# Optimization experiments

Measured on AMD Instinct MI355X. Metric: run time of the kernel, lower is better.

Reference implementation:

```python
import jax, jax.numpy as jnp
import numpy as np

B, S, D, H, FF = 2, 2048, 1024, 16, 4096
DK = D // H
MAX_SEQ_LEN = 2048
THETA = 10000.0
EPS = 1e-5


def _linear_init(key, out_f, in_f):
    std = (2.0 / (in_f + out_f)) ** 0.5
    return std * jax.random.truncated_normal(key, -3.0, 3.0, (out_f, in_f), dtype=jnp.float32)


def setup_inputs() -> dict:
    key = jax.random.key(0)
    ks = jax.random.split(key, 9)
    x = jax.random.normal(ks[0], (B, S, D), dtype=jnp.float32)
    token_positions = jnp.broadcast_to(jnp.arange(S, dtype=jnp.int32)[None, :], (B, S))
    return {
        "x": x,
        "wq": _linear_init(ks[1], D, D),
        "wk": _linear_init(ks[2], D, D),
        "wv": _linear_init(ks[3], D, D),
        "wo": _linear_init(ks[4], D, D),
        "w1": _linear_init(ks[5], FF, D),
        "w2": _linear_init(ks[6], D, FF),
        "w3": _linear_init(ks[7], FF, D),
        "g1": jnp.ones((D,), dtype=jnp.float32),
        "g2": jnp.ones((D,), dtype=jnp.float32),
        "token_positions": token_positions,
    }


def _rmsnorm(x, g):
    x32 = x.astype(jnp.float32)
    ms = jnp.sqrt(jnp.mean(x32 * x32, axis=-1, keepdims=True) + EPS)
    return ((x32 / ms) * g).astype(x.dtype)


def _rope(x, pos):
    # x: (B, H, S, DK); pos: (B, S)
    inv_freq = 1.0 / THETA ** (jnp.arange(0, DK, 2, dtype=jnp.float32) / DK)  # (DK/2,)
    freqs = pos.astype(jnp.float32)[..., None] * inv_freq  # (B, S, DK/2)
    cos = jnp.cos(freqs)[:, None, :, :]  # (B, 1, S, DK/2) broadcast over heads
    sin = jnp.sin(freqs)[:, None, :, :]
    x_real = x[..., 0::2]
    x_imag = x[..., 1::2]
    rot_real = x_real * cos - x_imag * sin
    rot_imag = x_real * sin + x_imag * cos
    return jnp.stack([rot_real, rot_imag], axis=-1).reshape(x.shape)


def reference(x, wq, wk, wv, wo, w1, w2, w3, g1, g2, token_positions):
    # --- attention sublayer ---
    h = _rmsnorm(x, g1)
    def proj(w):
        y = jnp.einsum('bsd,ed->bse', h, w)
        return y.reshape(B, S, H, DK).transpose(0, 2, 1, 3)  # (B,H,S,DK)
    Q = _rope(proj(wq), token_positions)
    K = _rope(proj(wk), token_positions)
    V = proj(wv)
    scores = jnp.einsum('bhqd,bhkd->bhqk', Q, K)  # (B,H,S,S) full matrix (naive)
    causal = jnp.tril(jnp.ones((S, S), dtype=bool))
    scores = jnp.where(causal, scores, -jnp.inf) / (DK ** 0.5)
    probs = jax.nn.softmax(scores, axis=-1)
    attn = jnp.einsum('bhqk,bhkd->bhqd', probs, V)
    attn = attn.transpose(0, 2, 1, 3).reshape(B, S, D)
    attn = jnp.einsum('bsd,ed->bse', attn, wo)
    y = x + attn
    # --- SwiGLU FFN sublayer ---
    h2 = _rmsnorm(y, g2)
    a = jnp.einsum('bsd,fd->bsf', h2, w1)
    gate = jnp.einsum('bsd,fd->bsf', h2, w3)
    ff = jnp.einsum('bsf,df->bsd', a * jax.nn.sigmoid(a) * gate, w2)
    return y + ff
```

## Files before the change

kernel.cpp:

```cpp
#include <hip/hip_runtime.h>
#include <hip/hip_bf16.h>

#define B_ 2
#define S_ 2048
#define D_ 1024
#define H_ 16
#define DK_ 64
#define FF_ 4096
#define M_ (B_ * S_)

typedef unsigned short u16;
typedef __bf16 bf16x8 __attribute__((ext_vector_type(8)));
typedef float f32x4 __attribute__((ext_vector_type(4)));
typedef u16 u16x4 __attribute__((ext_vector_type(4)));
typedef u16 u16x8 __attribute__((ext_vector_type(8)));

__device__ __forceinline__ u16 f2bf(float f) {
  __bf16 b = (__bf16)f;
  return __builtin_bit_cast(u16, b);
}
__device__ __forceinline__ float bf2f(u16 u) {
  __bf16 b = __builtin_bit_cast(__bf16, u);
  return (float)b;
}

__device__ __forceinline__ void async_lds16(const void* g, void* l) {
  __builtin_amdgcn_global_load_lds(
      (const __attribute__((address_space(1))) unsigned int*)g,
      (__attribute__((address_space(3))) unsigned int*)l, 16, 0, 0);
}

__global__ __launch_bounds__(256) void f2b_all(
    const float* __restrict__ wq, const float* __restrict__ wk,
    const float* __restrict__ wv, const float* __restrict__ wo,
    const float* __restrict__ w1, const float* __restrict__ w2,
    const float* __restrict__ w3, u16* __restrict__ wqkvb,
    u16* __restrict__ wob, u16* __restrict__ w1b, u16* __restrict__ w2b,
    u16* __restrict__ w3b) {
  int i4 = blockIdx.x * 256 + threadIdx.x;
  const float* src;
  u16* dst;
  int off;
  if (i4 < 262144) { src = wq; dst = wqkvb; off = i4; }
  else if (i4 < 524288) { src = wk; dst = wqkvb + 1048576; off = i4 - 262144; }
  else if (i4 < 786432) { src = wv; dst = wqkvb + 2097152; off = i4 - 524288; }
  else if (i4 < 1048576) { src = wo; dst = wob; off = i4 - 786432; }
  else if (i4 < 2097152) { src = w1; dst = w1b; off = i4 - 1048576; }
  else if (i4 < 3145728) { src = w2; dst = w2b; off = i4 - 2097152; }
  else { src = w3; dst = w3b; off = i4 - 3145728; }
  float4 v = ((const float4*)src)[off];
  u16x4 o;
  o[0] = f2bf(v.x); o[1] = f2bf(v.y); o[2] = f2bf(v.z); o[3] = f2bf(v.w);
  *(u16x4*)(dst + (size_t)off * 4) = o;
}

__global__ __launch_bounds__(256) void rmsnorm_k(const float* __restrict__ X,
                                                 const float* __restrict__ G,
                                                 u16* __restrict__ Out) {
  const int row = blockIdx.x, tid = threadIdx.x;
  const float4 xv = *(const float4*)(X + (size_t)row * D_ + tid * 4);
  float ss = xv.x * xv.x + xv.y * xv.y + xv.z * xv.z + xv.w * xv.w;
#pragma unroll
  for (int off = 1; off < 64; off <<= 1) ss += __shfl_xor(ss, off);
  __shared__ float red[4];
  if ((tid & 63) == 0) red[tid >> 6] = ss;
  __syncthreads();
  const float tot = red[0] + red[1] + red[2] + red[3];
  const float sc = rsqrtf(tot * (1.0f / D_) + 1e-5f);
  const float4 gv = *(const float4*)(G + tid * 4);
  u16x4 o;
  o[0] = f2bf(xv.x * sc * gv.x);
  o[1] = f2bf(xv.y * sc * gv.y);
  o[2] = f2bf(xv.z * sc * gv.z);
  o[3] = f2bf(xv.w * sc * gv.w);
  *(u16x4*)(Out + (size_t)row * D_ + tid * 4) = o;
}

__global__ __launch_bounds__(256) void rope2_k(unsigned int* __restrict__ Qb,
                                               unsigned int* __restrict__ Kb,
                                               const int* __restrict__ pos) {
  int idx = blockIdx.x * 256 + threadIdx.x;
  unsigned int* buf = Qb;
  float scale = 0.125f;
  if (idx >= 2097152) { buf = Kb; scale = 1.f; idx -= 2097152; }
  const int row = idx >> 9, p = idx & 511;
  const int i = p & 31;
  unsigned int v = buf[(size_t)row * 512 + p];
  const float xr = bf2f((u16)(v & 0xffffu));
  const float xi = bf2f((u16)(v >> 16));
  const float ang =
      (float)pos[row] * __expf(-(float)i * (9.210340371976184f / 32.0f));
  float sn, cs;
  sincosf(ang, &sn, &cs);
  const float orr = (xr * cs - xi * sn) * scale;
  const float oii = (xr * sn + xi * cs) * scale;
  buf[(size_t)row * 512 + p] =
      (unsigned int)f2bf(orr) | ((unsigned int)f2bf(oii) << 16);
}

__global__ __launch_bounds__(256) void transpose_v(const u16* __restrict__ V,
                                                   u16* __restrict__ Vt) {
  __shared__ __align__(16) u16 tile[32][64];
  const int tid = threadIdx.x;
  const int s0 = blockIdx.x * 32, bh = blockIdx.y, b = bh >> 4, h = bh & 15;
  {
    const int sr = tid >> 3, c = tid & 7;
    *(u16x8*)&tile[sr][c * 8] =
        *(const u16x8*)(V + (size_t)(b * S_ + s0 + sr) * D_ + h * DK_ + c * 8);
  }
  __syncthreads();
  {
    const int dk = tid >> 2, cs = tid & 3;
    u16x8 vv;
#pragma unroll
    for (int j = 0; j < 8; ++j) vv[j] = tile[cs * 8 + j][dk];
    *(u16x8*)(Vt + (size_t)(bh * DK_ + dk) * S_ + s0 + cs * 8) = vv;
  }
}

template <int BM, int BN, int BK, int EPI>
__global__ __launch_bounds__(512) void gemm2ph(const u16* __restrict__ A,
                                               const u16* __restrict__ Bw,
                                               void* __restrict__ Cout,
                                               const void* __restrict__ auxp,
                                               int N, int K) {
  constexpr int CPR = BK / 8;
  constexpr int ACH = BM * CPR;
  constexpr int TCH = (BM + BN) * CPR;
  constexpr int MR = BM / 32, NR = BN / 64;
  __shared__ __align__(16) u16 As[2][BM * BK];
  __shared__ __align__(16) u16 Bs[2][BN * BK];
  const int tid = threadIdx.x, l = tid & 63, w = tid >> 6;
  const int gx = gridDim.x;
  const int nwg = gx * (int)gridDim.y;
  const int id = blockIdx.y * gx + blockIdx.x;
  const int swz = (id & 7) * (nwg >> 3) + (id >> 3);
  const int m0 = (swz / gx) * BM, n0 = (swz % gx) * BN;
  const int wm = (w >> 2) * (BM / 2), wn = (w & 3) * (BN / 4);
  const int lr = l & 15, lg = l >> 4;

  f32x4 acc[MR][NR] = {};

  auto STAGE = [&](int bf, int k0) {
#pragma unroll
    for (int i = 0; i < TCH / 512; ++i) {
      const int s = i * 512 + tid;
      const int base = i * 512 + w * 64;
      if (base < ACH) {
        const int r = s / CPR, ch = s % CPR;
        async_lds16(A + (size_t)(m0 + r) * K + k0 + ((ch ^ (r & 7)) * 8),
                    (char*)As[bf] + base * 16);
      } else {
        const int s2 = s - ACH;
        const int r = s2 / CPR, ch = s2 % CPR;
        async_lds16(Bw + (size_t)(n0 + r) * K + k0 + ((ch ^ (r & 7)) * 8),
                    (char*)Bs[bf] + (base - ACH) * 16);
      }
    }
  };

  STAGE(0, 0);
  __syncthreads();
  int cur = 0;
  for (int k0 = 0; k0 < K; k0 += BK) {
    if (k0 + BK < K) STAGE(cur ^ 1, k0 + BK);
#pragma unroll
    for (int kk = 0; kk < BK / 32; ++kk) {
      bf16x8 af[MR], bfr[NR];
#pragma unroll
      for (int i = 0; i < MR; ++i) {
        const int row = wm + i * 16 + lr;
        af[i] = *(const bf16x8*)&As[cur][row * BK +
                                         (((kk * 4 + lg) ^ (row & 7)) * 8)];
      }
#pragma unroll
      for (int j = 0; j < NR; ++j) {
        const int row = wn + j * 16 + lr;
        bfr[j] = *(const bf16x8*)&Bs[cur][row * BK +
                                          (((kk * 4 + lg) ^ (row & 7)) * 8)];
      }
      __builtin_amdgcn_s_setprio(1);
#pragma unroll
      for (int i = 0; i < MR; ++i)
#pragma unroll
        for (int j = 0; j < NR; ++j)
          acc[i][j] = __builtin_amdgcn_mfma_f32_16x16x32_bf16(
              af[i], bfr[j], acc[i][j], 0, 0, 0);
      __builtin_amdgcn_s_setprio(0);
    }
    __syncthreads();
    cur ^= 1;
  }

#pragma unroll
  for (int i = 0; i < MR; ++i) {
#pragma unroll
    for (int j = 0; j < NR; ++j) {
#pragma unroll
      for (int t = 0; t < 4; ++t) {
        const int grow = m0 + wm + i * 16 + lg * 4 + t;
        const int gcol = n0 + wn + j * 16 + lr;
        const float v = acc[i][j][t];
        if (EPI == 0) {
          ((u16*)Cout)[(size_t)grow * N + gcol] = f2bf(v);
        } else if (EPI == 1) {
          const size_t idx = (size_t)grow * N + gcol;
          ((float*)Cout)[idx] = ((const float*)auxp)[idx] + v;
        } else if (EPI == 2) {
          const size_t idx = (size_t)grow * N + gcol;
          const float av = bf2f(((const u16*)auxp)[idx]);
          const float sw = av / (1.f + __expf(-av));
          ((u16*)Cout)[idx] = f2bf(sw * v);
        } else {
          u16* base = (u16*)Cout + (size_t)(gcol >> 10) * ((size_t)M_ * D_);
          base[(size_t)grow * D_ + (gcol & 1023)] = f2bf(v);
        }
      }
    }
  }
}

__global__ __launch_bounds__(256) void attn_fwd(const u16* __restrict__ Q,
                                                const u16* __restrict__ K,
                                                const u16* __restrict__ Vt,
                                                u16* __restrict__ O) {
  __shared__ __align__(16) u16 Ks[2][64 * 64];
  __shared__ __align__(16) u16 Vs[2][64 * 64];
  __shared__ __align__(16) u16 Ps[4][16 * 72];
  const int tid = threadIdx.x, l = tid & 63, w = tid >> 6;
  const int lr = l & 15, lg = l >> 4;
  const int bid = blockIdx.x;
  const int xcd = bid & 7, i = bid >> 3;
  const int bh = xcd * 4 + (i >> 5);
  const int qx = 31 - (i & 31);
  const int b = bh >> 4, h = bh & 15;
  const int q0w = qx * 64 + w * 16;

  const u16* Kb = K + (size_t)(b * S_) * D_ + h * DK_;
  const u16* Vb = Vt + (size_t)bh * DK_ * S_;

  bf16x8 aq[2];
  {
    const u16* qp = Q + (size_t)(b * S_ + q0w + lr) * D_ + h * DK_ + lg * 8;
    aq[0] = *(const bf16x8*)qp;
    aq[1] = *(const bf16x8*)(qp + 32);
  }
  f32x4 oacc[4] = {};
  float mrow[4], lrow[4];
#pragma unroll
  for (int t = 0; t < 4; ++t) { mrow[t] = -1e30f; lrow[t] = 0.f; }

  auto STAGE = [&](int bf, int t) {
#pragma unroll
    for (int inst = 0; inst < 2; ++inst) {
      const int s = (w * 2 + inst) * 64 + l;
      const int r = s >> 3, ch = s & 7;
      const int chs = ch ^ (r & 7);
      async_lds16(Kb + (size_t)(t * 64 + r) * D_ + chs * 8,
                  (char*)Ks[bf] + (w * 2 + inst) * 1024);
      async_lds16(Vb + (size_t)r * S_ + t * 64 + chs * 8,
                  (char*)Vs[bf] + (w * 2 + inst) * 1024);
    }
  };

  auto QKT = [&](int cur, f32x4* sf) {
    __builtin_amdgcn_s_setprio(1);
#pragma unroll
    for (int n = 0; n < 4; ++n) {
      const int kvr = n * 16 + lr;
      f32x4 z = {};
#pragma unroll
      for (int ss = 0; ss < 2; ++ss) {
        const int cw = ss * 4 + lg;
        bf16x8 bk = *(const bf16x8*)&Ks[cur][kvr * 64 + ((cw ^ (kvr & 7)) * 8)];
        z = __builtin_amdgcn_mfma_f32_16x16x32_bf16(aq[ss], bk, z, 0, 0, 0);
      }
      sf[n] = z;
    }
    __builtin_amdgcn_s_setprio(0);
  };

  auto PV = [&](int cur) {
    bf16x8 ap0 = *(const bf16x8*)&Ps[w][lr * 72 + lg * 8];
    bf16x8 ap1 = *(const bf16x8*)&Ps[w][lr * 72 + 32 + lg * 8];
    __builtin_amdgcn_s_setprio(1);
#pragma unroll
    for (int d = 0; d < 4; ++d) {
      const int row = d * 16 + lr;
      bf16x8 bv0 = *(const bf16x8*)&Vs[cur][row * 64 + ((lg ^ (row & 7)) * 8)];
      bf16x8 bv1 =
          *(const bf16x8*)&Vs[cur][row * 64 + (((4 + lg) ^ (row & 7)) * 8)];
      oacc[d] = __builtin_amdgcn_mfma_f32_16x16x32_bf16(ap0, bv0, oacc[d], 0, 0, 0);
      oacc[d] = __builtin_amdgcn_mfma_f32_16x16x32_bf16(ap1, bv1, oacc[d], 0, 0, 0);
    }
    __builtin_amdgcn_s_setprio(0);
  };

  STAGE(0, 0);
  __syncthreads();
  int cur = 0;
  for (int it = 0; it < qx; ++it) {
    STAGE(cur ^ 1, it + 1);
    f32x4 sf[4];
    QKT(cur, sf);
    float fm[4];
    bool exc = false;
#pragma unroll
    for (int t = 0; t < 4; ++t) {
      fm[t] = fmaxf(fmaxf(sf[0][t], sf[1][t]), fmaxf(sf[2][t], sf[3][t]));
      exc |= fm[t] > mrow[t] + 8.f;
    }
    if (__any(exc)) {
#pragma unroll
      for (int t = 0; t < 4; ++t) {
        float mx = fm[t];
#pragma unroll
        for (int off = 1; off < 16; off <<= 1)
          mx = fmaxf(mx, __shfl_xor(mx, off));
        const float nm = fmaxf(mrow[t], mx);
        const float c = __expf(mrow[t] - nm);
        mrow[t] = nm;
        lrow[t] *= c;
#pragma unroll
        for (int d = 0; d < 4; ++d) oacc[d][t] *= c;
      }
    }
#pragma unroll
    for (int t = 0; t < 4; ++t) {
      float ps = 0.f;
#pragma unroll
      for (int n = 0; n < 4; ++n) {
        const float e = __expf(sf[n][t] - mrow[t]);
        ps += e;
        Ps[w][(lg * 4 + t) * 72 + n * 16 + lr] = f2bf(e);
      }
#pragma unroll
      for (int off = 1; off < 16; off <<= 1) ps += __shfl_xor(ps, off);
      lrow[t] += ps;
    }
    PV(cur);
    __syncthreads();
    cur ^= 1;
  }
  {
    const int kv0 = qx * 64;
    f32x4 sf[4];
    QKT(cur, sf);
#pragma unroll
    for (int t = 0; t < 4; ++t) {
      const int qrow = q0w + lg * 4 + t;
      float v[4];
#pragma unroll
      for (int n = 0; n < 4; ++n)
        v[n] = (kv0 + n * 16 + lr <= qrow) ? sf[n][t] : -1e30f;
      float mx = fmaxf(fmaxf(v[0], v[1]), fmaxf(v[2], v[3]));
#pragma unroll
      for (int off = 1; off < 16; off <<= 1) mx = fmaxf(mx, __shfl_xor(mx, off));
      const float nm = fmaxf(mrow[t], mx);
      float e[4], ps = 0.f;
#pragma unroll
      for (int n = 0; n < 4; ++n) { e[n] = __expf(v[n] - nm); ps += e[n]; }
#pragma unroll
      for (int off = 1; off < 16; off <<= 1) ps += __shfl_xor(ps, off);
      const float c = __expf(mrow[t] - nm);
      lrow[t] = lrow[t] * c + ps;
      mrow[t] = nm;
#pragma unroll
      for (int d = 0; d < 4; ++d) oacc[d][t] *= c;
#pragma unroll
      for (int n = 0; n < 4; ++n)
        Ps[w][(lg * 4 + t) * 72 + n * 16 + lr] = f2bf(e[n]);
    }
    PV(cur);
  }
#pragma unroll
  for (int d = 0; d < 4; ++d) {
#pragma unroll
    for (int t = 0; t < 4; ++t) {
      const size_t idx =
          (size_t)(b * S_ + q0w + lg * 4 + t) * D_ + h * DK_ + d * 16 + lr;
      O[idx] = f2bf(oacc[d][t] / lrow[t]);
    }
  }
}

extern "C" void kernel_launch(void* const* d_in, const int* in_sizes, int n_in,
                              void* d_out, int out_size, void* d_ws,
                              size_t ws_size, hipStream_t stream) {
  (void)in_sizes; (void)n_in; (void)out_size; (void)ws_size;
  const float* x = (const float*)d_in[0];
  const float* wq = (const float*)d_in[1];
  const float* wk = (const float*)d_in[2];
  const float* wv = (const float*)d_in[3];
  const float* wo = (const float*)d_in[4];
  const float* w1 = (const float*)d_in[5];
  const float* w2 = (const float*)d_in[6];
  const float* w3 = (const float*)d_in[7];
  const float* g1 = (const float*)d_in[8];
  const float* g2 = (const float*)d_in[9];
  const int* tp = (const int*)d_in[10];
  float* out = (float*)d_out;

  char* ws = (char*)d_ws;
  const size_t MB = 1024u * 1024u;
  u16* wqkvb = (u16*)(ws + 0 * MB);
  u16* wob = (u16*)(ws + 6 * MB);
  u16* w1b = (u16*)(ws + 8 * MB);
  u16* w2b = (u16*)(ws + 16 * MB);
  u16* w3b = (u16*)(ws + 24 * MB);
  u16* hb  = (u16*)(ws + 32 * MB);
  float* yb = (float*)(ws + 40 * MB);
  u16* h2b = (u16*)(ws + 56 * MB);
  u16* Qb  = (u16*)(ws + 64 * MB);
  u16* Kb  = (u16*)(ws + 72 * MB);
  u16* Vb  = (u16*)(ws + 80 * MB);
  u16* Vtb = (u16*)(ws + 88 * MB);
  u16* ab  = (u16*)(ws + 64 * MB);
  u16* ffb = (u16*)(ws + 96 * MB);
  u16* aob = hb;

  f2b_all<<<16384, 256, 0, stream>>>(wq, wk, wv, wo, w1, w2, w3, wqkvb, wob,
                                     w1b, w2b, w3b);

  rmsnorm_k<<<4096, 256, 0, stream>>>(x, g1, hb);

  gemm2ph<256, 256, 64, 3><<<dim3(12, 16), 512, 0, stream>>>(
      hb, wqkvb, Qb, nullptr, 3072, 1024);

  rope2_k<<<16384, 256, 0, stream>>>((unsigned int*)Qb, (unsigned int*)Kb, tp);
  transpose_v<<<dim3(64, 32), 256, 0, stream>>>(Vb, Vtb);

  attn_fwd<<<1024, 256, 0, stream>>>(Qb, Kb, Vtb, aob);

  gemm2ph<128, 128, 128, 1><<<dim3(8, 32), 512, 0, stream>>>(aob, wob, yb, x,
                                                             1024, 1024);
  rmsnorm_k<<<4096, 256, 0, stream>>>(yb, g2, h2b);

  gemm2ph<256, 256, 64, 0><<<dim3(16, 16), 512, 0, stream>>>(
      h2b, w1b, ab, nullptr, 4096, 1024);
  gemm2ph<256, 256, 64, 2><<<dim3(16, 16), 512, 0, stream>>>(h2b, w3b, ffb, ab,
                                                             4096, 1024);
  gemm2ph<128, 128, 128, 1><<<dim3(8, 32), 512, 0, stream>>>(ffb, w2b, out, yb,
                                                             1024, 4096);
}
```

Before: 303.8 us.

## Fuse RoPE and V transpose into QKV GEMM epilogue; widen attention query tiles

Measured after the change: 782.8 us. 2.58x slower.

```diff
diff --git a/kernel.cpp b/kernel.cpp
--- a/kernel.cpp
+++ b/kernel.cpp
@@ -76,54 +76,13 @@
   *(u16x4*)(Out + (size_t)row * D_ + tid * 4) = o;
 }
 
-__global__ __launch_bounds__(256) void rope2_k(unsigned int* __restrict__ Qb,
-                                               unsigned int* __restrict__ Kb,
-                                               const int* __restrict__ pos) {
-  int idx = blockIdx.x * 256 + threadIdx.x;
-  unsigned int* buf = Qb;
-  float scale = 0.125f;
-  if (idx >= 2097152) { buf = Kb; scale = 1.f; idx -= 2097152; }
-  const int row = idx >> 9, p = idx & 511;
-  const int i = p & 31;
-  unsigned int v = buf[(size_t)row * 512 + p];
-  const float xr = bf2f((u16)(v & 0xffffu));
-  const float xi = bf2f((u16)(v >> 16));
-  const float ang =
-      (float)pos[row] * __expf(-(float)i * (9.210340371976184f / 32.0f));
-  float sn, cs;
-  sincosf(ang, &sn, &cs);
-  const float orr = (xr * cs - xi * sn) * scale;
-  const float oii = (xr * sn + xi * cs) * scale;
-  buf[(size_t)row * 512 + p] =
-      (unsigned int)f2bf(orr) | ((unsigned int)f2bf(oii) << 16);
-}
-
-__global__ __launch_bounds__(256) void transpose_v(const u16* __restrict__ V,
-                                                   u16* __restrict__ Vt) {
-  __shared__ __align__(16) u16 tile[32][64];
-  const int tid = threadIdx.x;
-  const int s0 = blockIdx.x * 32, bh = blockIdx.y, b = bh >> 4, h = bh & 15;
-  {
-    const int sr = tid >> 3, c = tid & 7;
-    *(u16x8*)&tile[sr][c * 8] =
-        *(const u16x8*)(V + (size_t)(b * S_ + s0 + sr) * D_ + h * DK_ + c * 8);
-  }
-  __syncthreads();
-  {
-    const int dk = tid >> 2, cs = tid & 3;
-    u16x8 vv;
-#pragma unroll
-    for (int j = 0; j < 8; ++j) vv[j] = tile[cs * 8 + j][dk];
-    *(u16x8*)(Vt + (size_t)(bh * DK_ + dk) * S_ + s0 + cs * 8) = vv;
-  }
-}
-
 template <int BM, int BN, int BK, int EPI>
 __global__ __launch_bounds__(512) void gemm2ph(const u16* __restrict__ A,
                                                const u16* __restrict__ Bw,
                                                void* __restrict__ Cout,
                                                const void* __restrict__ auxp,
-                                               int N, int K) {
+                                               int N, int K,
+                                               const int* __restrict__ tp) {
   constexpr int CPR = BK / 8;
   constexpr int ACH = BM * CPR;
   constexpr int TCH = (BM + BN) * CPR;
@@ -192,28 +151,73 @@
     cur ^= 1;
   }
 
-#pragma unroll
-  for (int i = 0; i < MR; ++i) {
-#pragma unroll
-    for (int j = 0; j < NR; ++j) {
-#pragma unroll
-      for (int t = 0; t < 4; ++t) {
-        const int grow = m0 + wm + i * 16 + lg * 4 + t;
-        const int gcol = n0 + wn + j * 16 + lr;
-        const float v = acc[i][j][t];
-        if (EPI == 0) {
-          ((u16*)Cout)[(size_t)grow * N + gcol] = f2bf(v);
-        } else if (EPI == 1) {
-          const size_t idx = (size_t)grow * N + gcol;
-          ((float*)Cout)[idx] = ((const float*)auxp)[idx] + v;
-        } else if (EPI == 2) {
-          const size_t idx = (size_t)grow * N + gcol;
-          const float av = bf2f(((const u16*)auxp)[idx]);
-          const float sw = av / (1.f + __expf(-av));
-          ((u16*)Cout)[idx] = f2bf(sw * v);
-        } else {
-          u16* base = (u16*)Cout + (size_t)(gcol >> 10) * ((size_t)M_ * D_);
-          base[(size_t)grow * D_ + (gcol & 1023)] = f2bf(v);
+  if (EPI != 3) {
+#pragma unroll
+    for (int i = 0; i < MR; ++i) {
+#pragma unroll
+      for (int j = 0; j < NR; ++j) {
+#pragma unroll
+        for (int t = 0; t < 4; ++t) {
+          const int grow = m0 + wm + i * 16 + lg * 4 + t;
+          const int gcol = n0 + wn + j * 16 + lr;
+          const float v = acc[i][j][t];
+          if (EPI == 0) {
+            ((u16*)Cout)[(size_t)grow * N + gcol] = f2bf(v);
+          } else if (EPI == 1) {
+            const size_t idx = (size_t)grow * N + gcol;
+            ((float*)Cout)[idx] = ((const float*)auxp)[idx] + v;
+          } else if (EPI == 2) {
+            const size_t idx = (size_t)grow * N + gcol;
+            const float av = bf2f(((const u16*)auxp)[idx]);
+            const float sw = av / (1.f + __expf(-av));
+            ((u16*)Cout)[idx] = f2bf(sw * v);
+          }
+        }
+      }
+    }
+  } else {
+    const int region = n0 >> 10;
+    if (region < 2) {
+      u16* dst = (u16*)Cout + (size_t)region * ((size_t)M_ * D_);
+      const float qscale = (region == 0) ? 0.125f : 1.0f;
+#pragma unroll
+      for (int i = 0; i < MR; ++i) {
+        const int grow0 = m0 + wm + i * 16 + lg * 4;
+        float posf[4];
+#pragma unroll
+        for (int t = 0; t < 4; ++t) posf[t] = (float)tp[grow0 + t];
+#pragma unroll
+        for (int j = 0; j < NR; ++j) {
+          const int gcol = n0 + wn + j * 16 + lr;
+          const float invf = __expf(-(float)((gcol & 63) >> 1) *
+                                    (9.210340371976184f / 32.0f));
+          const float sgn = (gcol & 1) ? 1.f : -1.f;
+#pragma unroll
+          for (int t = 0; t < 4; ++t) {
+            const float own = acc[i][j][t];
+            const float pe = __shfl_xor(own, 1);
+            float sn, cs;
+            sincosf(posf[t] * invf, &sn, &cs);
+            dst[(size_t)(grow0 + t) * D_ + (gcol & 1023)] =
+                f2bf((own * cs + sgn * pe * sn) * qscale);
+          }
+        }
+      }
+    } else {
+      u16* vt = (u16*)Cout + 2 * ((size_t)M_ * D_);
+#pragma unroll
+      for (int i = 0; i < MR; ++i) {
+        const int grow0 = m0 + wm + i * 16 + lg * 4;
+        const int bb = grow0 >> 11, s0 = grow0 & 2047;
+#pragma unroll
+        for (int j = 0; j < NR; ++j) {
+          const int vcol = (n0 + wn + j * 16 + lr) & 1023;
+          u16x4 pk;
+#pragma unroll
+          for (int t = 0; t < 4; ++t) pk[t] = f2bf(acc[i][j][t]);
+          const size_t addr =
+              ((size_t)(bb * 16 + (vcol >> 6)) * 64 + (vcol & 63)) * 2048 + s0;
+          *(u16x4*)(vt + addr) = pk;
         }
       }
     }
@@ -226,29 +230,41 @@
                                                 u16* __restrict__ O) {
   __shared__ __align__(16) u16 Ks[2][64 * 64];
   __shared__ __align__(16) u16 Vs[2][64 * 64];
-  __shared__ __align__(16) u16 Ps[4][16 * 72];
+  __shared__ __align__(16) u16 Ps[4][32 * 72];
   const int tid = threadIdx.x, l = tid & 63, w = tid >> 6;
   const int lr = l & 15, lg = l >> 4;
   const int bid = blockIdx.x;
   const int xcd = bid & 7, i = bid >> 3;
-  const int bh = xcd * 4 + (i >> 5);
-  const int qx = 31 - (i & 31);
+  const int bh = xcd * 4 + (i >> 4);
+  const int qx = 15 - (i & 15);
   const int b = bh >> 4, h = bh & 15;
-  const int q0w = qx * 64 + w * 16;
+  const int q0w = qx * 128 + w * 32;
 
   const u16* Kb = K + (size_t)(b * S_) * D_ + h * DK_;
   const u16* Vb = Vt + (size_t)bh * DK_ * S_;
 
-  bf16x8 aq[2];
-  {
-    const u16* qp = Q + (size_t)(b * S_ + q0w + lr) * D_ + h * DK_ + lg * 8;
-    aq[0] = *(const bf16x8*)qp;
-    aq[1] = *(const bf16x8*)(qp + 32);
+  bf16x8 aq[2][2];
+#pragma unroll
+  for (int g = 0; g < 2; ++g) {
+    const u16* qp =
+        Q + (size_t)(b * S_ + q0w + g * 16 + lr) * D_ + h * DK_ + lg * 8;
+    aq[g][0] = *(const bf16x8*)qp;
+    aq[g][1] = *(const bf16x8*)(qp + 32);
   }
-  f32x4 oacc[4] = {};
-  float mrow[4], lrow[4];
-#pragma unroll
-  for (int t = 0; t < 4; ++t) { mrow[t] = -1e30f; lrow[t] = 0.f; }
+  f32x4 oacc[2][4] = {};
+  float mrow[2][4], lrow[2][4];
+#pragma unroll
+  for (int g = 0; g < 2; ++g)
+#pragma unroll
+    for (int t = 0; t < 4; ++t) { mrow[g][t] = -1e30f; lrow[g][t] = 0.f; }
+
+  u16x8 ones_u;
+#pragma unroll
+  for (int j = 0; j < 8; ++j) ones_u[j] = 0x3F80;
+  const bf16x8 ones = __builtin_bit_cast(bf16x8, ones_u);
+
+  const int ntiles = qx * 2 + 2;
+  const int F = qx * 2 + (w >> 1);
 
   auto STAGE = [&](int bf, int t) {
 #pragma unroll
@@ -263,125 +279,123 @@
     }
   };
 
-  auto QKT = [&](int cur, f32x4* sf) {
-    __builtin_amdgcn_s_setprio(1);
-#pragma unroll
-    for (int n = 0; n < 4; ++n) {
-      const int kvr = n * 16 + lr;
-      f32x4 z = {};
-#pragma unroll
-      for (int ss = 0; ss < 2; ++ss) {
-        const int cw = ss * 4 + lg;
-        bf16x8 bk = *(const bf16x8*)&Ks[cur][kvr * 64 + ((cw ^ (kvr & 7)) * 8)];
-        z = __builtin_amdgcn_mfma_f32_16x16x32_bf16(aq[ss], bk, z, 0, 0, 0);
-      }
-      sf[n] = z;
-    }
-    __builtin_amdgcn_s_setprio(0);
-  };
-
-  auto PV = [&](int cur) {
-    bf16x8 ap0 = *(const bf16x8*)&Ps[w][lr * 72 + lg * 8];
-    bf16x8 ap1 = *(const bf16x8*)&Ps[w][lr * 72 + 32 + lg * 8];
-    __builtin_amdgcn_s_setprio(1);
-#pragma unroll
-    for (int d = 0; d < 4; ++d) {
-      const int row = d * 16 + lr;
-      bf16x8 bv0 = *(const bf16x8*)&Vs[cur][row * 64 + ((lg ^ (row & 7)) * 8)];
-      bf16x8 bv1 =
-          *(const bf16x8*)&Vs[cur][row * 64 + (((4 + lg) ^ (row & 7)) * 8)];
-      oacc[d] = __builtin_amdgcn_mfma_f32_16x16x32_bf16(ap0, bv0, oacc[d], 0, 0, 0);
-      oacc[d] = __builtin_amdgcn_mfma_f32_16x16x32_bf16(ap1, bv1, oacc[d], 0, 0, 0);
-    }
-    __builtin_amdgcn_s_setprio(0);
-  };
-
   STAGE(0, 0);
   __syncthreads();
   int cur = 0;
-  for (int it = 0; it < qx; ++it) {
-    STAGE(cur ^ 1, it + 1);
-    f32x4 sf[4];
-    QKT(cur, sf);
-    float fm[4];
-    bool exc = false;
-#pragma unroll
-    for (int t = 0; t < 4; ++t) {
-      fm[t] = fmaxf(fmaxf(sf[0][t], sf[1][t]), fmaxf(sf[2][t], sf[3][t]));
-      exc |= fm[t] > mrow[t] + 8.f;
-    }
-    if (__any(exc)) {
-#pragma unroll
-      for (int t = 0; t < 4; ++t) {
-        float mx = fm[t];
-#pragma unroll
-        for (int off = 1; off < 16; off <<= 1)
-          mx = fmaxf(mx, __shfl_xor(mx, off));
-        const float nm = fmaxf(mrow[t], mx);
-        const float c = __expf(mrow[t] - nm);
-        mrow[t] = nm;
-        lrow[t] *= c;
-#pragma unroll
-        for (int d = 0; d < 4; ++d) oacc[d][t] *= c;
-      }
-    }
-#pragma unroll
-    for (int t = 0; t < 4; ++t) {
-      float ps = 0.f;
-#pragma unroll
-      for (int n = 0; n < 4; ++n) {
-        const float e = __expf(sf[n][t] - mrow[t]);
-        ps += e;
-        Ps[w][(lg * 4 + t) * 72 + n * 16 + lr] = f2bf(e);
-      }
-#pragma unroll
-      for (int off = 1; off < 16; off <<= 1) ps += __shfl_xor(ps, off);
-      lrow[t] += ps;
-    }
-    PV(cur);
+  for (int it = 0; it < ntiles; ++it) {
+    if (it + 1 < ntiles) STAGE(cur ^ 1, it + 1);
+    if (it <= F) {
+      const bool diag = (it == F);
+#pragma unroll
+      for (int g = 0; g < 2; ++g) {
+        f32x4 sf[4];
+        __builtin_amdgcn_s_setprio(1);
+#pragma unroll
+        for (int n = 0; n < 4; ++n) {
+          const int kvr = n * 16 + lr;
+          f32x4 z = {};
+          bf16x8 bk0 = *(const bf16x8*)&Ks[cur][kvr * 64 + ((lg ^ (kvr & 7)) * 8)];
+          bf16x8 bk1 =
+              *(const bf16x8*)&Ks[cur][kvr * 64 + (((4 + lg) ^ (kvr & 7)) * 8)];
+          z = __builtin_amdgcn_mfma_f32_16x16x32_bf16(aq[g][0], bk0, z, 0, 0, 0);
+          z = __builtin_amdgcn_mfma_f32_16x16x32_bf16(aq[g][1], bk1, z, 0, 0, 0);
+          sf[n] = z;
+        }
+        __builtin_amdgcn_s_setprio(0);
+        if (!diag) {
+          float fm[4];
+          bool exc = false;
+#pragma unroll
+          for (int t = 0; t < 4; ++t) {
+            fm[t] = fmaxf(fmaxf(sf[0][t], sf[1][t]), fmaxf(sf[2][t], sf[3][t]));
+            exc |= fm[t] > mrow[g][t] + 8.f;
+          }
+          if (__any(exc)) {
+#pragma unroll
+            for (int t = 0; t < 4; ++t) {
+              float mx = fm[t];
+#pragma unroll
+              for (int off = 1; off < 16; off <<= 1)
+                mx = fmaxf(mx, __shfl_xor(mx, off));
+              const float nm = fmaxf(mrow[g][t], mx);
+              const float c = __expf(mrow[g][t] - nm);
+              mrow[g][t] = nm;
+              lrow[g][t] *= c;
+#pragma unroll
+              for (int d = 0; d < 4; ++d) oacc[g][d][t] *= c;
+            }
+          }
+#pragma unroll
+          for (int t = 0; t < 4; ++t)
+#pragma unroll
+            for (int n = 0; n < 4; ++n)
+              Ps[w][(g * 16 + lg * 4 + t) * 72 + n * 16 + lr] =
+                  f2bf(__expf(sf[n][t] - mrow[g][t]));
+        } else {
+          const int kv0 = it * 64;
+#pragma unroll
+          for (int t = 0; t < 4; ++t) {
+            const int qrow = q0w + g * 16 + lg * 4 + t;
+            float v[4];
+#pragma unroll
+            for (int n = 0; n < 4; ++n)
+              v[n] = (kv0 + n * 16 + lr <= qrow) ? sf[n][t] : -1e30f;
+            float mx = fmaxf(fmaxf(v[0], v[1]), fmaxf(v[2], v[3]));
+#pragma unroll
+            for (int off = 1; off < 16; off <<= 1)
+              mx = fmaxf(mx, __shfl_xor(mx, off));
+            const float nm = fmaxf(mrow[g][t], mx);
+            const float c = __expf(mrow[g][t] - nm);
+            mrow[g][t] = nm;
+            lrow[g][t] *= c;
+#pragma unroll
+            for (int d = 0; d < 4; ++d) oacc[g][d][t] *= c;
+#pragma unroll
+            for (int n = 0; n < 4; ++n)
+              Ps[w][(g * 16 + lg * 4 + t) * 72 + n * 16 + lr] =
+                  f2bf(__expf(v[n] - nm));
+          }
+        }
+      }
+      __builtin_amdgcn_s_setprio(1);
+#pragma unroll
+      for (int g = 0; g < 2; ++g) {
+        bf16x8 ap0 = *(const bf16x8*)&Ps[w][(g * 16 + lr) * 72 + lg * 8];
+        bf16x8 ap1 = *(const bf16x8*)&Ps[w][(g * 16 + lr) * 72 + 32 + lg * 8];
+        f32x4 z = {};
+        z = __builtin_amdgcn_mfma_f32_16x16x32_bf16(ap0, ones, z, 0, 0, 0);
+        z = __builtin_amdgcn_mfma_f32_16x16x32_bf16(ap1, ones, z, 0, 0, 0);
+#pragma unroll
+        for (int d = 0; d < 4; ++d) {
+          const int row = d * 16 + lr;
+          bf16x8 bv0 =
+              *(const bf16x8*)&Vs[cur][row * 64 + ((lg ^ (row & 7)) * 8)];
+          bf16x8 bv1 =
+              *(const bf16x8*)&Vs[cur][row * 64 + (((4 + lg) ^ (row & 7)) * 8)];
+          oacc[g][d] = __builtin_amdgcn_mfma_f32_16x16x32_bf16(ap0, bv0,
+                                                               oacc[g][d], 0, 0, 0);
+          oacc[g][d] = __builtin_amdgcn_mfma_f32_16x16x32_bf16(ap1, bv1,
+                                                               oacc[g][d], 0, 0, 0);
+        }
+#pragma unroll
+        for (int t = 0; t < 4; ++t) lrow[g][t] += z[t];
+      }
+      __builtin_amdgcn_s_setprio(0);
+    }
     __syncthreads();
     cur ^= 1;
   }
-  {
-    const int kv0 = qx * 64;
-    f32x4 sf[4];
-    QKT(cur, sf);
-#pragma unroll
-    for (int t = 0; t < 4; ++t) {
-      const int qrow = q0w + lg * 4 + t;
-      float v[4];
-#pragma unroll
-      for (int n = 0; n < 4; ++n)
-        v[n] = (kv0 + n * 16 + lr <= qrow) ? sf[n][t] : -1e30f;
-      float mx = fmaxf(fmaxf(v[0], v[1]), fmaxf(v[2], v[3]));
-#pragma unroll
-      for (int off = 1; off < 16; off <<= 1) mx = fmaxf(mx, __shfl_xor(mx, off));
-      const float nm = fmaxf(mrow[t], mx);
-      float e[4], ps = 0.f;
-#pragma unroll
-      for (int n = 0; n < 4; ++n) { e[n] = __expf(v[n] - nm); ps += e[n]; }
-#pragma unroll
-      for (int off = 1; off < 16; off <<= 1) ps += __shfl_xor(ps, off);
-      const float c = __expf(mrow[t] - nm);
-      lrow[t] = lrow[t] * c + ps;
-      mrow[t] = nm;
-#pragma unroll
-      for (int d = 0; d < 4; ++d) oacc[d][t] *= c;
-#pragma unroll
-      for (int n = 0; n < 4; ++n)
-        Ps[w][(lg * 4 + t) * 72 + n * 16 + lr] = f2bf(e[n]);
-    }
-    PV(cur);
-  }
-#pragma unroll
-  for (int d = 0; d < 4; ++d) {
-#pragma unroll
-    for (int t = 0; t < 4; ++t) {
-      const size_t idx =
-          (size_t)(b * S_ + q0w + lg * 4 + t) * D_ + h * DK_ + d * 16 + lr;
-      O[idx] = f2bf(oacc[d][t] / lrow[t]);
-    }
-  }
+#pragma unroll
+  for (int g = 0; g < 2; ++g)
+#pragma unroll
+    for (int d = 0; d < 4; ++d)
+#pragma unroll
+      for (int t = 0; t < 4; ++t) {
+        const size_t idx =
+            (size_t)(b * S_ + q0w + g * 16 + lg * 4 + t) * D_ + h * DK_ +
+            d * 16 + lr;
+        O[idx] = f2bf(oacc[g][d][t] / lrow[g][t]);
+      }
 }
 
 extern "C" void kernel_launch(void* const* d_in, const int* in_sizes, int n_in,
@@ -413,8 +427,7 @@
   u16* h2b = (u16*)(ws + 56 * MB);
   u16* Qb  = (u16*)(ws + 64 * MB);
   u16* Kb  = (u16*)(ws + 72 * MB);
-  u16* Vb  = (u16*)(ws + 80 * MB);
-  u16* Vtb = (u16*)(ws + 88 * MB);
+  u16* Vtb = (u16*)(ws + 80 * MB);
   u16* ab  = (u16*)(ws + 64 * MB);
   u16* ffb = (u16*)(ws + 96 * MB);
   u16* aob = hb;
@@ -425,21 +438,18 @@
   rmsnorm_k<<<4096, 256, 0, stream>>>(x, g1, hb);
 
   gemm2ph<256, 256, 64, 3><<<dim3(12, 16), 512, 0, stream>>>(
-      hb, wqkvb, Qb, nullptr, 3072, 1024);
-
-  rope2_k<<<16384, 256, 0, stream>>>((unsigned int*)Qb, (unsigned int*)Kb, tp);
-  transpose_v<<<dim3(64, 32), 256, 0, stream>>>(Vb, Vtb);
-
-  attn_fwd<<<1024, 256, 0, stream>>>(Qb, Kb, Vtb, aob);
-
-  gemm2ph<128, 128, 128, 1><<<dim3(8, 32), 512, 0, stream>>>(aob, wob, yb, x,
-                                                             1024, 1024);
+      hb, wqkvb, Qb, nullptr, 3072, 1024, tp);
+
+  attn_fwd<<<512, 256, 0, stream>>>(Qb, Kb, Vtb, aob);
+
+  gemm2ph<128, 128, 128, 1><<<dim3(8, 32), 512, 0, stream>>>(
+      aob, wob, yb, x, 1024, 1024, nullptr);
   rmsnorm_k<<<4096, 256, 0, stream>>>(yb, g2, h2b);
 
   gemm2ph<256, 256, 64, 0><<<dim3(16, 16), 512, 0, stream>>>(
-      h2b, w1b, ab, nullptr, 4096, 1024);
-  gemm2ph<256, 256, 64, 2><<<dim3(16, 16), 512, 0, stream>>>(h2b, w3b, ffb, ab,
-                                                             4096, 1024);
-  gemm2ph<128, 128, 128, 1><<<dim3(8, 32), 512, 0, stream>>>(ffb, w2b, out, yb,
-                                                             1024, 4096);
-}
+      h2b, w1b, ab, nullptr, 4096, 1024, nullptr);
+  gemm2ph<256, 256, 64, 2><<<dim3(16, 16), 512, 0, stream>>>(
+      h2b, w3b, ffb, ab, 4096, 1024, nullptr);
+  gemm2ph<128, 128, 128, 1><<<dim3(8, 32), 512, 0, stream>>>(
+      ffb, w2b, out, yb, 1024, 4096, nullptr);
+}
```

## Use vmcnt-based partial waits in GEMM and MFMA row-sums in attention

Applied to the files above, without the earlier changes.

Result: faster. 292.6 us (-3.7%).

```diff
diff --git a/kernel.cpp b/kernel.cpp
--- a/kernel.cpp
+++ b/kernel.cpp
@@ -29,6 +29,11 @@
       (const __attribute__((address_space(1))) unsigned int*)g,
       (__attribute__((address_space(3))) unsigned int*)l, 16, 0, 0);
 }
+
+__device__ __forceinline__ void raw_barrier() {
+  asm volatile("s_barrier" ::: "memory");
+}
+#define VMCNT_WAIT(n) asm volatile("s_waitcnt vmcnt(" #n ")" ::: "memory")
 
 __global__ __launch_bounds__(256) void f2b_all(
     const float* __restrict__ wq, const float* __restrict__ wk,
@@ -128,6 +133,7 @@
   constexpr int ACH = BM * CPR;
   constexpr int TCH = (BM + BN) * CPR;
   constexpr int MR = BM / 32, NR = BN / 64;
+  static_assert(TCH / 512 == 8, "vmcnt(8) assumes 8 loads/thread per STAGE");
   __shared__ __align__(16) u16 As[2][BM * BK];
   __shared__ __align__(16) u16 Bs[2][BN * BK];
   const int tid = threadIdx.x, l = tid & 63, w = tid >> 6;
@@ -160,10 +166,15 @@
   };
 
   STAGE(0, 0);
-  __syncthreads();
   int cur = 0;
   for (int k0 = 0; k0 < K; k0 += BK) {
-    if (k0 + BK < K) STAGE(cur ^ 1, k0 + BK);
+    if (k0 + BK < K) {
+      STAGE(cur ^ 1, k0 + BK);
+      VMCNT_WAIT(8);
+    } else {
+      VMCNT_WAIT(0);
+    }
+    raw_barrier();
 #pragma unroll
     for (int kk = 0; kk < BK / 32; ++kk) {
       bf16x8 af[MR], bfr[NR];
@@ -188,7 +199,7 @@
               af[i], bfr[j], acc[i][j], 0, 0, 0);
       __builtin_amdgcn_s_setprio(0);
     }
-    __syncthreads();
+    raw_barrier();
     cur ^= 1;
   }
 
@@ -250,6 +261,13 @@
 #pragma unroll
   for (int t = 0; t < 4; ++t) { mrow[t] = -1e30f; lrow[t] = 0.f; }
 
+  u16x8 ones_u;
+#pragma unroll
+  for (int j = 0; j < 8; ++j) ones_u[j] = 0x3F80;
+  const bf16x8 ones = __builtin_bit_cast(bf16x8, ones_u);
+
+  const int ntiles = qx + 1;
+
   auto STAGE = [&](int bf, int t) {
 #pragma unroll
     for (int inst = 0; inst < 2; ++inst) {
@@ -263,27 +281,84 @@
     }
   };
 
-  auto QKT = [&](int cur, f32x4* sf) {
+  STAGE(0, 0);
+  __syncthreads();
+  int cur = 0;
+  for (int it = 0; it < ntiles; ++it) {
+    if (it + 1 < ntiles) STAGE(cur ^ 1, it + 1);
+    f32x4 sf[4];
     __builtin_amdgcn_s_setprio(1);
 #pragma unroll
     for (int n = 0; n < 4; ++n) {
       const int kvr = n * 16 + lr;
       f32x4 z = {};
-#pragma unroll
-      for (int ss = 0; ss < 2; ++ss) {
-        const int cw = ss * 4 + lg;
-        bf16x8 bk = *(const bf16x8*)&Ks[cur][kvr * 64 + ((cw ^ (kvr & 7)) * 8)];
-        z = __builtin_amdgcn_mfma_f32_16x16x32_bf16(aq[ss], bk, z, 0, 0, 0);
-      }
+      bf16x8 bk0 = *(const bf16x8*)&Ks[cur][kvr * 64 + ((lg ^ (kvr & 7)) * 8)];
+      bf16x8 bk1 =
+          *(const bf16x8*)&Ks[cur][kvr * 64 + (((4 + lg) ^ (kvr & 7)) * 8)];
+      z = __builtin_amdgcn_mfma_f32_16x16x32_bf16(aq[0], bk0, z, 0, 0, 0);
+      z = __builtin_amdgcn_mfma_f32_16x16x32_bf16(aq[1], bk1, z, 0, 0, 0);
       sf[n] = z;
     }
     __builtin_amdgcn_s_setprio(0);
-  };
-
-  auto PV = [&](int cur) {
+    if (it < qx) {
+      float fm[4];
+      bool exc = false;
+#pragma unroll
+      for (int t = 0; t < 4; ++t) {
+        fm[t] = fmaxf(fmaxf(sf[0][t], sf[1][t]), fmaxf(sf[2][t], sf[3][t]));
+        exc |= fm[t] > mrow[t] + 8.f;
+      }
+      if (__any(exc)) {
+#pragma unroll
+        for (int t = 0; t < 4; ++t) {
+          float mx = fm[t];
+#pragma unroll
+          for (int off = 1; off < 16; off <<= 1)
+            mx = fmaxf(mx, __shfl_xor(mx, off));
+          const float nm = fmaxf(mrow[t], mx);
+          const float c = __expf(mrow[t] - nm);
+          mrow[t] = nm;
+          lrow[t] *= c;
+#pragma unroll
+          for (int d = 0; d < 4; ++d) oacc[d][t] *= c;
+        }
+      }
+#pragma unroll
+      for (int t = 0; t < 4; ++t)
+#pragma unroll
+        for (int n = 0; n < 4; ++n)
+          Ps[w][(lg * 4 + t) * 72 + n * 16 + lr] =
+              f2bf(__expf(sf[n][t] - mrow[t]));
+    } else {
+      const int kv0 = it * 64;
+#pragma unroll
+      for (int t = 0; t < 4; ++t) {
+        const int qrow = q0w + lg * 4 + t;
+        float v[4];
+#pragma unroll
+        for (int n = 0; n < 4; ++n)
+          v[n] = (kv0 + n * 16 + lr <= qrow) ? sf[n][t] : -1e30f;
+        float mx = fmaxf(fmaxf(v[0], v[1]), fmaxf(v[2], v[3]));
+#pragma unroll
+        for (int off = 1; off < 16; off <<= 1)
+          mx = fmaxf(mx, __shfl_xor(mx, off));
+        const float nm = fmaxf(mrow[t], mx);
+        const float c = __expf(mrow[t] - nm);
+        mrow[t] = nm;
+        lrow[t] *= c;
+#pragma unroll
+        for (int d = 0; d < 4; ++d) oacc[d][t] *= c;
+#pragma unroll
+        for (int n = 0; n < 4; ++n)
+          Ps[w][(lg * 4 + t) * 72 + n * 16 + lr] = f2bf(__expf(v[n] - nm));
+      }
+    }
     bf16x8 ap0 = *(const bf16x8*)&Ps[w][lr * 72 + lg * 8];
     bf16x8 ap1 = *(const bf16x8*)&Ps[w][lr * 72 + 32 + lg * 8];
     __builtin_amdgcn_s_setprio(1);
+    f32x4 zs = {};
+    zs = __builtin_amdgcn_mfma_f32_16x16x32_bf16(ap0, ones, zs, 0, 0, 0);
+    zs = __builtin_amdgcn_mfma_f32_16x16x32_bf16(ap1, ones, zs, 0, 0, 0);
 #pragma unroll
     for (int d = 0; d < 4; ++d) {
       const int row = d * 16 + lr;
@@ -294,84 +369,10 @@
       oacc[d] = __builtin_amdgcn_mfma_f32_16x16x32_bf16(ap1, bv1, oacc[d], 0, 0, 0);
     }
     __builtin_amdgcn_s_setprio(0);
-  };
-
-  STAGE(0, 0);
-  __syncthreads();
-  int cur = 0;
-  for (int it = 0; it < qx; ++it) {
-    STAGE(cur ^ 1, it + 1);
-    f32x4 sf[4];
-    QKT(cur, sf);
-    float fm[4];
-    bool exc = false;
-#pragma unroll
-    for (int t = 0; t < 4; ++t) {
-      fm[t] = fmaxf(fmaxf(sf[0][t], sf[1][t]), fmaxf(sf[2][t], sf[3][t]));
-      exc |= fm[t] > mrow[t] + 8.f;
-    }
-    if (__any(exc)) {
-#pragma unroll
-      for (int t = 0; t < 4; ++t) {
-        float mx = fm[t];
-#pragma unroll
-        for (int off = 1; off < 16; off <<= 1)
-          mx = fmaxf(mx, __shfl_xor(mx, off));
-        const float nm = fmaxf(mrow[t], mx);
-        const float c = __expf(mrow[t] - nm);
-        mrow[t] = nm;
-        lrow[t] *= c;
-#pragma unroll
-        for (int d = 0; d < 4; ++d) oacc[d][t] *= c;
-      }
-    }
-#pragma unroll
-    for (int t = 0; t < 4; ++t) {
-      float ps = 0.f;
-#pragma unroll
-      for (int n = 0; n < 4; ++n) {
-        const float e = __expf(sf[n][t] - mrow[t]);
-        ps += e;
-        Ps[w][(lg * 4 + t) * 72 + n * 16 + lr] = f2bf(e);
-      }
-#pragma unroll
-      for (int off = 1; off < 16; off <<= 1) ps += __shfl_xor(ps, off);
-      lrow[t] += ps;
-    }
-    PV(cur);
+#pragma unroll
+    for (int t = 0; t < 4; ++t) lrow[t] += zs[t];
     __syncthreads();
     cur ^= 1;
-  }
-  {
-    const int kv0 = qx * 64;
-    f32x4 sf[4];
-    QKT(cur, sf);
-#pragma unroll
-    for (int t = 0; t < 4; ++t) {
-      const int qrow = q0w + lg * 4 + t;
-      float v[4];
-#pragma unroll
-      for (int n = 0; n < 4; ++n)
-        v[n] = (kv0 + n * 16 + lr <= qrow) ? sf[n][t] : -1e30f;
-      float mx = fmaxf(fmaxf(v[0], v[1]), fmaxf(v[2], v[3]));
-#pragma unroll
-      for (int off = 1; off < 16; off <<= 1) mx = fmaxf(mx, __shfl_xor(mx, off));
-      const float nm = fmaxf(mrow[t], mx);
-      float e[4], ps = 0.f;
-#pragma unroll
-      for (int n = 0; n < 4; ++n) { e[n] = __expf(v[n] - nm); ps += e[n]; }
-#pragma unroll
-      for (int off = 1; off < 16; off <<= 1) ps += __shfl_xor(ps, off);
-      const float c = __expf(mrow[t] - nm);
-      lrow[t] = lrow[t] * c + ps;
-      mrow[t] = nm;
-#pragma unroll
-      for (int d = 0; d < 4; ++d) oacc[d][t] *= c;
-#pragma unroll
-      for (int n = 0; n < 4; ++n)
-        Ps[w][(lg * 4 + t) * 72 + n * 16 + lr] = f2bf(e[n]);
-    }
-    PV(cur);
   }
 #pragma unroll
   for (int d = 0; d < 4; ++d) {
```
